# Performance work log

Measured on AMD Instinct MI355X. Metric: run time of the kernel, lower is better.

Reference implementation:

```python
import jax, jax.numpy as jnp
import numpy as np

D_K = 24
ALPHA = 0.1
N_HEADS = 6
D_MODEL = 144
LN_EPS = 1e-5


def setup_inputs() -> dict:
    key = jax.random.key(0)
    ks = jax.random.split(key, 8)
    B, S = 8, 2048
    Q = jax.random.normal(ks[0], (B, S, D_MODEL), dtype=jnp.float32)
    K = jax.random.normal(ks[1], (B, N_HEADS, S, D_K), dtype=jnp.float32)
    V = jax.random.normal(ks[2], (B, N_HEADS, S, D_K), dtype=jnp.float32)
    attn_mask = jax.random.randint(ks[3], (B, S, S), 0, 2).astype(bool)
    Wq_w = jax.random.normal(ks[4], (D_MODEL, D_MODEL), dtype=jnp.float32) * 0.05
    Wq_b = jnp.zeros((D_MODEL,), dtype=jnp.float32)
    lin_w = jax.random.normal(ks[5], (D_MODEL, D_MODEL), dtype=jnp.float32) * 0.05
    lin_b = jnp.zeros((D_MODEL,), dtype=jnp.float32)
    ln_g = jnp.ones((D_MODEL,), dtype=jnp.float32)
    ln_b = jnp.zeros((D_MODEL,), dtype=jnp.float32)
    return {"Q": Q, "K": K, "V": V, "attn_mask": attn_mask,
            "Wq_w": Wq_w, "Wq_b": Wq_b, "lin_w": lin_w, "lin_b": lin_b,
            "ln_g": ln_g, "ln_b": ln_b}


def reference(Q, K, V, attn_mask, Wq_w, Wq_b, lin_w, lin_b, ln_g, ln_b):
    B, S, _ = Q.shape
    residual = Q
    # W_Q projection then head split: [B,S,D] -> [B,H,S,d_k]
    q = (Q @ Wq_w.T + Wq_b).reshape(B, S, N_HEADS, D_K).transpose(0, 2, 1, 3)
    # scores [B,H,S,Sk]; custom tanh activation instead of softmax
    scores = jnp.einsum('bhqd,bhkd->bhqk', q, K) / np.sqrt(D_K).astype(np.float32)
    attn = jnp.tanh(ALPHA * scores)
    # NOTE: original calls attn.masked_fill(...) non-inplace and drops the
    # result, so attn_mask has no effect. Faithfully ignored here.
    context = jnp.einsum('bhqk,bhkd->bhqd', attn, V)
    context = context.transpose(0, 2, 1, 3).reshape(B, S, N_HEADS * D_K)
    output = context @ lin_w.T + lin_b
    x = output + residual
    mu = jnp.mean(x, axis=-1, keepdims=True)
    var = jnp.var(x, axis=-1, keepdims=True)
    return (x - mu) / jnp.sqrt(var + LN_EPS) * ln_g + ln_b
```

## Files before the change

kernel.cpp:

```cpp
#include <hip/hip_runtime.h>
#include <hip/hip_bf16.h>

#define B_  8
#define S_  2048
#define H_  6
#define DK_ 24
#define DM_ 144

#define TK0  2.0412414523193153e-02f
#define TK1 -2.8350575726379381e-06f
#define TK2  4.7250959543965635e-10f

typedef __bf16 bf16x8 __attribute__((ext_vector_type(8)));
typedef __bf16 bf16x2 __attribute__((ext_vector_type(2)));
typedef float  f32x4  __attribute__((ext_vector_type(4)));

#define MFMA_ __builtin_amdgcn_mfma_f32_16x16x32_bf16

__device__ __forceinline__ unsigned short f2bf(float f) {
    return __builtin_bit_cast(unsigned short, (__bf16)f);
}
__device__ __forceinline__ uint pack2(float a, float b) {
    bf16x2 v; v[0] = (__bf16)a; v[1] = (__bf16)b;
    return __builtin_bit_cast(uint, v);
}
__device__ __forceinline__ float tanh_s(float c) {
    float t = c * c;
    float u = fmaf(t, TK2, TK1);
    u = fmaf(t, u, TK0);
    return c * u;
}

__global__ __launch_bounds__(256)
void prep_w_kernel(const float* __restrict__ Wq, const float* __restrict__ Wqb,
                   const float* __restrict__ Wl, const float* __restrict__ lb,
                   ushort* __restrict__ Whq, ushort* __restrict__ Wlp) {
    int i = blockIdx.x * 256 + threadIdx.x;
    if (i < 30720) {
        int h = i / 5120, rem = i % 5120;
        int d = rem / 160, c = rem % 160;
        float v = 0.f;
        if (d < DK_) {
            if (c < DM_)       v = Wq[(h * DK_ + d) * DM_ + c];
            else if (c == DM_) v = Wqb[h * DK_ + d];
        }
        Whq[i] = f2bf(v);
    } else if (i < 53760) {
        int j = i - 30720;
        int r = j / 160, c = j % 160;
        float v = (c < DM_) ? Wl[r * DM_ + c] : (c == DM_ ? lb[r] : 0.f);
        Wlp[j] = f2bf(v);
    }
}

__global__ __launch_bounds__(256)
void prep_kv_kernel(const float* __restrict__ K, const float* __restrict__ V,
                    ushort* __restrict__ Ktt, ushort* __restrict__ Vtt) {
    __shared__ float sv[64 * 25];
    const int t = threadIdx.x;
    const int kt = blockIdx.x, h = blockIdx.y, b = blockIdx.z;
    const int bh = b * H_ + h;
    const size_t tile = (size_t)(bh * 32 + kt);
    const float4* Ks = (const float4*)(K + ((size_t)bh * S_ + kt * 64) * DK_);
    ushort* Ko = Ktt + tile * 2048;
    for (int idx = t; idx < 384; idx += 256) {
        int r = idx / 6, c4 = (idx % 6) * 4;
        float4 v = Ks[idx];
        ushort4 u; u.x = f2bf(v.x); u.y = f2bf(v.y); u.z = f2bf(v.z); u.w = f2bf(v.w);
        *(ushort4*)&Ko[r * 32 + c4] = u;
    }
    if (t < 64) { uint4 z = {0u,0u,0u,0u}; *(uint4*)&Ko[t * 32 + 24] = z; }
    const float4* Vs = (const float4*)(V + ((size_t)bh * S_ + kt * 64) * DK_);
    for (int idx = t; idx < 384; idx += 256) {
        int r = idx / 6, c4 = (idx % 6) * 4;
        *(float4*)&sv[r * 25 + c4] = Vs[idx];
    }
    __syncthreads();
    int d = t >> 3, s8 = (t & 7) * 8;
    uint4 o = {0u,0u,0u,0u};
    if (d < DK_) {
        o.x = pack2(sv[(s8 + 0) * 25 + d], sv[(s8 + 1) * 25 + d]);
        o.y = pack2(sv[(s8 + 2) * 25 + d], sv[(s8 + 3) * 25 + d]);
        o.z = pack2(sv[(s8 + 4) * 25 + d], sv[(s8 + 5) * 25 + d]);
        o.w = pack2(sv[(s8 + 6) * 25 + d], sv[(s8 + 7) * 25 + d]);
    }
    ((uint4*)Vtt)[tile * 256 + t] = o;
}

__global__ __launch_bounds__(512, 6)
void attn_kernel(const float* __restrict__ Q, const ushort* __restrict__ Whq,
                 const ushort* __restrict__ Ktt, const ushort* __restrict__ Vtt,
                 float* __restrict__ out) {
    __shared__ __attribute__((aligned(16))) char smem[48128];
    ushort* s_q  = (ushort*)smem;
    ushort* s_k  = (ushort*)(smem + 10240);
    ushort* s_vt = (ushort*)(smem + 20480);
    ushort* s_p  = (ushort*)(smem + 29696);
    float*  s_ctx = (float*)smem;

    const int t = threadIdx.x;
    const int w = t >> 6, n16 = t & 15, g = (t >> 4) & 3;
    const int qp = blockIdx.x, h = blockIdx.y, b = blockIdx.z;
    const int bh = b * H_ + h;
    const int row0 = qp * 128;

    const uint4* Kb4 = (const uint4*)Ktt + (size_t)bh * 8192;
    const uint4* Vb4 = (const uint4*)Vtt + (size_t)bh * 8192;

    const int t2 = t & 255;
    const int stoff = (t < 256) ? ((t2 >> 2) * 40 + (t2 & 3) * 8)
                                : ((t2 >> 3) * 72 + (t2 & 7) * 8);
    uint4 sreg = (t < 256) ? Kb4[t2] : Vb4[t2];

    const f32x4 zf = {0.f, 0.f, 0.f, 0.f};
    const uint4* Wh4 = (const uint4*)Whq + h * 640;
    {
        const float* Qr = Q + (size_t)(b * S_ + row0 + w * 16 + n16) * DM_;
        f32x4 qa0 = zf, qa1 = zf;
#pragma unroll
        for (int ks = 0; ks < 5; ++ks) {
            bf16x8 av;
            if (ks < 4 || g < 2) {
                float4 f0 = *(const float4*)&Qr[ks * 32 + g * 8];
                float4 f1 = *(const float4*)&Qr[ks * 32 + g * 8 + 4];
                uint4 u;
                u.x = pack2(f0.x, f0.y); u.y = pack2(f0.z, f0.w);
                u.z = pack2(f1.x, f1.y); u.w = pack2(f1.z, f1.w);
                av = __builtin_bit_cast(bf16x8, u);
            } else {
                uint4 u = {0u, 0u, 0u, 0u};
                if (g == 2) u.x = 0x00003F80u;
                av = __builtin_bit_cast(bf16x8, u);
            }
            bf16x8 bv0 = __builtin_bit_cast(bf16x8, Wh4[n16 * 20 + ks * 4 + g]);
            bf16x8 bv1 = __builtin_bit_cast(bf16x8, Wh4[(16 + n16) * 20 + ks * 4 + g]);
            qa0 = MFMA_(av, bv0, qa0, 0, 0, 0);
            qa1 = MFMA_(av, bv1, qa1, 0, 0, 0);
        }
#pragma unroll
        for (int reg = 0; reg < 4; ++reg) {
            int r = (w * 16 + g * 4 + reg) * 40;
            s_q[r + n16]      = f2bf(qa0[reg]);
            s_q[r + 16 + n16] = f2bf(qa1[reg]);
        }
    }
    const bf16x8 qf = *(const bf16x8*)&s_q[(w * 16 + n16) * 40 + g * 8];

    ushort* s_pw = s_p + w * 1152;
    const int prow = n16 * 72;
    f32x4 acc0 = zf, acc1 = zf;
    int p = 0;
    for (int kt = 0; kt < 32; ++kt) {
        if (t < 256) *(uint4*)&s_k[p * 2560 + stoff] = sreg;
        else         *(uint4*)&s_vt[p * 2304 + stoff] = sreg;
        __syncthreads();
        {
            int nt = ((kt + 1) & 31) * 256;
            sreg = (t < 256) ? Kb4[nt + t2] : Vb4[nt + t2];
        }
        bf16x8 a0 = *(const bf16x8*)&s_k[p * 2560 + n16 * 40 + g * 8];
        bf16x8 a1 = *(const bf16x8*)&s_k[p * 2560 + (16 + n16) * 40 + g * 8];
        bf16x8 a2 = *(const bf16x8*)&s_k[p * 2560 + (32 + n16) * 40 + g * 8];
        bf16x8 a3 = *(const bf16x8*)&s_k[p * 2560 + (48 + n16) * 40 + g * 8];
        f32x4 c0 = MFMA_(a0, qf, zf, 0, 0, 0);
        f32x4 c1 = MFMA_(a1, qf, zf, 0, 0, 0);
        f32x4 c2 = MFMA_(a2, qf, zf, 0, 0, 0);
        f32x4 c3 = MFMA_(a3, qf, zf, 0, 0, 0);
        uint2 u;
        u.x = pack2(tanh_s(c0[0]), tanh_s(c0[1]));
        u.y = pack2(tanh_s(c0[2]), tanh_s(c0[3]));
        *(uint2*)&s_pw[prow + 0  + g * 4] = u;
        u.x = pack2(tanh_s(c1[0]), tanh_s(c1[1]));
        u.y = pack2(tanh_s(c1[2]), tanh_s(c1[3]));
        *(uint2*)&s_pw[prow + 16 + g * 4] = u;
        u.x = pack2(tanh_s(c2[0]), tanh_s(c2[1]));
        u.y = pack2(tanh_s(c2[2]), tanh_s(c2[3]));
        *(uint2*)&s_pw[prow + 32 + g * 4] = u;
        u.x = pack2(tanh_s(c3[0]), tanh_s(c3[1]));
        u.y = pack2(tanh_s(c3[2]), tanh_s(c3[3]));
        *(uint2*)&s_pw[prow + 48 + g * 4] = u;
        bf16x8 ap0 = *(const bf16x8*)&s_pw[prow + g * 8];
        bf16x8 ap1 = *(const bf16x8*)&s_pw[prow + 32 + g * 8];
        bf16x8 vb00 = *(const bf16x8*)&s_vt[p * 2304 + n16 * 72 + g * 8];
        bf16x8 vb01 = *(const bf16x8*)&s_vt[p * 2304 + n16 * 72 + 32 + g * 8];
        bf16x8 vb10 = *(const bf16x8*)&s_vt[p * 2304 + (16 + n16) * 72 + g * 8];
        bf16x8 vb11 = *(const bf16x8*)&s_vt[p * 2304 + (16 + n16) * 72 + 32 + g * 8];
        acc0 = MFMA_(ap0, vb00, acc0, 0, 0, 0);
        acc0 = MFMA_(ap1, vb01, acc0, 0, 0, 0);
        acc1 = MFMA_(ap0, vb10, acc1, 0, 0, 0);
        acc1 = MFMA_(ap1, vb11, acc1, 0, 0, 0);
        p ^= 1;
    }

    __syncthreads();
#pragma unroll
    for (int reg = 0; reg < 4; ++reg) {
        int row = w * 16 + g * 4 + reg;
        s_ctx[row * 28 + n16] = acc0[reg];
        if (n16 < 8) s_ctx[row * 28 + 16 + n16] = acc1[reg];
    }
    __syncthreads();
    for (int idx = t; idx < 768; idx += 512) {
        int r = idx / 6, c = idx % 6;
        float4 v4 = *(const float4*)&s_ctx[r * 28 + c * 4];
        *(float4*)&out[((size_t)b * S_ + row0 + r) * DM_ + h * DK_ + c * 4] = v4;
    }
}

__global__ __launch_bounds__(512)
void outln_kernel(const float* __restrict__ Qres, const ushort* __restrict__ Wlp,
                  const float* __restrict__ lg, const float* __restrict__ lbeta,
                  float* __restrict__ io) {
    __shared__ __attribute__((aligned(16))) ushort s_a[64 * 168];
    __shared__ __attribute__((aligned(16))) ushort s_w[144 * 168];
    __shared__ float s_red[2][2][64];
    const int t = threadIdx.x;
    const int w = t >> 6, n16 = t & 15, g = (t >> 4) & 3;
    const int wq = w & 3, half = w >> 2;
    const int nt_base = half * 5, nt_cnt = half ? 4 : 5;
    const int row0 = blockIdx.x * 64;

    for (int idx = t; idx < 2304; idx += 512) {
        int r = idx / 36, c4 = (idx % 36) * 4;
        float4 v = *(const float4*)&io[(size_t)(row0 + r) * DM_ + c4];
        uint2 u; u.x = pack2(v.x, v.y); u.y = pack2(v.z, v.w);
        *(uint2*)&s_a[r * 168 + c4] = u;
    }
    if (t < 64) {
        uint4 pad = {0x00003F80u, 0u, 0u, 0u};
        uint4 z4  = {0u, 0u, 0u, 0u};
        *(uint4*)&s_a[t * 168 + 144] = pad;
        *(uint4*)&s_a[t * 168 + 152] = z4;
    }
    for (int idx = t; idx < 2880; idx += 512) {
        int r = idx / 20, c8 = (idx % 20) * 8;
        *(uint4*)&s_w[r * 168 + c8] = *(const uint4*)&Wlp[r * 160 + c8];
    }
    __syncthreads();

    f32x4 acc[5];
#pragma unroll
    for (int j = 0; j < 5; ++j) acc[j] = (f32x4){0.f, 0.f, 0.f, 0.f};
#pragma unroll
    for (int ks = 0; ks < 5; ++ks) {
        bf16x8 av = *(const bf16x8*)&s_a[(wq * 16 + n16) * 168 + ks * 32 + g * 8];
        for (int j = 0; j < nt_cnt; ++j) {
            bf16x8 bv = *(const bf16x8*)&s_w[((nt_base + j) * 16 + n16) * 168 + ks * 32 + g * 8];
            acc[j] = MFMA_(av, bv, acc[j], 0, 0, 0);
        }
    }
    float vals[5][4], s1[4] = {0, 0, 0, 0}, s2[4] = {0, 0, 0, 0};
    for (int j = 0; j < nt_cnt; ++j) {
        int d = (nt_base + j) * 16 + n16;
#pragma unroll
        for (int reg = 0; reg < 4; ++reg) {
            int row = row0 + wq * 16 + g * 4 + reg;
            float v = acc[j][reg] + Qres[(size_t)row * DM_ + d];
            vals[j][reg] = v;
            s1[reg] += v; s2[reg] = fmaf(v, v, s2[reg]);
        }
    }
#pragma unroll
    for (int off = 1; off < 16; off <<= 1) {
#pragma unroll
        for (int reg = 0; reg < 4; ++reg) {
            s1[reg] += __shfl_xor(s1[reg], off);
            s2[reg] += __shfl_xor(s2[reg], off);
        }
    }
    if (n16 == 0) {
#pragma unroll
        for (int reg = 0; reg < 4; ++reg) {
            int rr = wq * 16 + g * 4 + reg;
            s_red[half][0][rr] = s1[reg];
            s_red[half][1][rr] = s2[reg];
        }
    }
    __syncthreads();
    float mu[4], rs[4];
#pragma unroll
    for (int reg = 0; reg < 4; ++reg) {
        int rr = wq * 16 + g * 4 + reg;
        float S1 = s_red[0][0][rr] + s_red[1][0][rr];
        float S2 = s_red[0][1][rr] + s_red[1][1][rr];
        float m = S1 * (1.f / 144.f);
        mu[reg] = m;
        rs[reg] = rsqrtf(S2 * (1.f / 144.f) - m * m + 1e-5f);
    }
    for (int j = 0; j < nt_cnt; ++j) {
        int d = (nt_base + j) * 16 + n16;
        float gv = lg[d], bv = lbeta[d];
#pragma unroll
        for (int reg = 0; reg < 4; ++reg) {
            int row = row0 + wq * 16 + g * 4 + reg;
            io[(size_t)row * DM_ + d] = (vals[j][reg] - mu[reg]) * rs[reg] * gv + bv;
        }
    }
}

extern "C" void kernel_launch(void* const* d_in, const int* in_sizes, int n_in,
                              void* d_out, int out_size, void* d_ws, size_t ws_size,
                              hipStream_t stream) {
    const float* Q     = (const float*)d_in[0];
    const float* K     = (const float*)d_in[1];
    const float* V     = (const float*)d_in[2];
    const float* Wq_w  = (const float*)d_in[4];
    const float* Wq_b  = (const float*)d_in[5];
    const float* lin_w = (const float*)d_in[6];
    const float* lin_b = (const float*)d_in[7];
    const float* ln_g  = (const float*)d_in[8];
    const float* ln_b  = (const float*)d_in[9];
    float* out = (float*)d_out;

    ushort* Ktt = (ushort*)d_ws;
    ushort* Vtt = (ushort*)((char*)d_ws + 6291456);
    ushort* Whq = (ushort*)((char*)d_ws + 12582912);
    ushort* Wlp = (ushort*)((char*)d_ws + 12644352);

    prep_w_kernel<<<210, 256, 0, stream>>>(Wq_w, Wq_b, lin_w, lin_b, Whq, Wlp);
    prep_kv_kernel<<<dim3(32, H_, B_), 256, 0, stream>>>(K, V, Ktt, Vtt);
    attn_kernel<<<dim3(S_ / 128, H_, B_), 512, 0, stream>>>(Q, Whq, Ktt, Vtt, out);
    outln_kernel<<<(B_ * S_) / 64, 512, 0, stream>>>(Q, Wlp, ln_g, ln_b, out);
}
```

Measured before the change: 268.4 us.

## Split attention key range across waves with LDS atomic reduction, drop shared K/V staging

```diff
diff --git a/kernel.cpp b/kernel.cpp
--- a/kernel.cpp
+++ b/kernel.cpp
@@ -87,32 +87,31 @@
     ((uint4*)Vtt)[tile * 256 + t] = o;
 }
 
-__global__ __launch_bounds__(512, 6)
+__global__ __launch_bounds__(256, 3)
 void attn_kernel(const float* __restrict__ Q, const ushort* __restrict__ Whq,
                  const ushort* __restrict__ Ktt, const ushort* __restrict__ Vtt,
                  float* __restrict__ out) {
-    __shared__ __attribute__((aligned(16))) char smem[48128];
+    __shared__ __attribute__((aligned(16))) char smem[51200];
     ushort* s_q  = (ushort*)smem;
-    ushort* s_k  = (ushort*)(smem + 10240);
-    ushort* s_vt = (ushort*)(smem + 20480);
-    ushort* s_p  = (ushort*)(smem + 29696);
-    float*  s_ctx = (float*)smem;
+    float*  s_ctx = (float*)(smem + 5120);
 
     const int t = threadIdx.x;
     const int w = t >> 6, n16 = t & 15, g = (t >> 4) & 3;
     const int qp = blockIdx.x, h = blockIdx.y, b = blockIdx.z;
     const int bh = b * H_ + h;
-    const int row0 = qp * 128;
+    const int row0 = qp * 64;
 
     const uint4* Kb4 = (const uint4*)Ktt + (size_t)bh * 8192;
     const uint4* Vb4 = (const uint4*)Vtt + (size_t)bh * 8192;
-
-    const int t2 = t & 255;
-    const int stoff = (t < 256) ? ((t2 >> 2) * 40 + (t2 & 3) * 8)
-                                : ((t2 >> 3) * 72 + (t2 & 7) * 8);
-    uint4 sreg = (t < 256) ? Kb4[t2] : Vb4[t2];
-
+    const int koff = n16 * 4 + g;
+    const int voff = n16 * 8 + g;
     const f32x4 zf = {0.f, 0.f, 0.f, 0.f};
+
+    bf16x8 kf[4];
+#pragma unroll
+    for (int mt = 0; mt < 4; ++mt)
+        kf[mt] = __builtin_bit_cast(bf16x8, Kb4[w * 256 + mt * 64 + koff]);
+
     const uint4* Wh4 = (const uint4*)Whq + h * 640;
     {
         const float* Qr = Q + (size_t)(b * S_ + row0 + w * 16 + n16) * DM_;
@@ -144,65 +143,75 @@
             s_q[r + 16 + n16] = f2bf(qa1[reg]);
         }
     }
-    const bf16x8 qf = *(const bf16x8*)&s_q[(w * 16 + n16) * 40 + g * 8];
-
-    ushort* s_pw = s_p + w * 1152;
-    const int prow = n16 * 72;
-    f32x4 acc0 = zf, acc1 = zf;
-    int p = 0;
-    for (int kt = 0; kt < 32; ++kt) {
-        if (t < 256) *(uint4*)&s_k[p * 2560 + stoff] = sreg;
-        else         *(uint4*)&s_vt[p * 2304 + stoff] = sreg;
-        __syncthreads();
+    for (int i = t; i < 2304; i += 256) s_ctx[i] = 0.f;
+    __syncthreads();
+
+    bf16x8 qf[4];
+#pragma unroll
+    for (int j = 0; j < 4; ++j)
+        qf[j] = *(const bf16x8*)&s_q[(j * 16 + n16) * 40 + g * 8];
+
+    ushort* s_pw = (ushort*)(smem + 14336) + w * 4608;
+    f32x4 acc[4][2];
+#pragma unroll
+    for (int m = 0; m < 4; ++m) { acc[m][0] = zf; acc[m][1] = zf; }
+
+    for (int i = 0; i < 8; ++i) {
+        const int kt = i * 4 + w;
+        uint4 vl[4];
+#pragma unroll
+        for (int j = 0; j < 4; ++j)
+            vl[j] = Vb4[kt * 256 + (j >> 1) * 128 + (j & 1) * 4 + voff];
+#pragma unroll
+        for (int mt = 0; mt < 4; ++mt) {
+            f32x4 c0 = MFMA_(kf[mt], qf[0], zf, 0, 0, 0);
+            f32x4 c1 = MFMA_(kf[mt], qf[1], zf, 0, 0, 0);
+            f32x4 c2 = MFMA_(kf[mt], qf[2], zf, 0, 0, 0);
+            f32x4 c3 = MFMA_(kf[mt], qf[3], zf, 0, 0, 0);
+            uint2 u;
+            u.x = pack2(tanh_s(c0[0]), tanh_s(c0[1]));
+            u.y = pack2(tanh_s(c0[2]), tanh_s(c0[3]));
+            *(uint2*)&s_pw[n16 * 72 + mt * 16 + g * 4] = u;
+            u.x = pack2(tanh_s(c1[0]), tanh_s(c1[1]));
+            u.y = pack2(tanh_s(c1[2]), tanh_s(c1[3]));
+            *(uint2*)&s_pw[(16 + n16) * 72 + mt * 16 + g * 4] = u;
+            u.x = pack2(tanh_s(c2[0]), tanh_s(c2[1]));
+            u.y = pack2(tanh_s(c2[2]), tanh_s(c2[3]));
+            *(uint2*)&s_pw[(32 + n16) * 72 + mt * 16 + g * 4] = u;
+            u.x = pack2(tanh_s(c3[0]), tanh_s(c3[1]));
+            u.y = pack2(tanh_s(c3[2]), tanh_s(c3[3]));
+            *(uint2*)&s_pw[(48 + n16) * 72 + mt * 16 + g * 4] = u;
+        }
         {
-            int nt = ((kt + 1) & 31) * 256;
-            sreg = (t < 256) ? Kb4[nt + t2] : Vb4[nt + t2];
-        }
-        bf16x8 a0 = *(const bf16x8*)&s_k[p * 2560 + n16 * 40 + g * 8];
-        bf16x8 a1 = *(const bf16x8*)&s_k[p * 2560 + (16 + n16) * 40 + g * 8];
-        bf16x8 a2 = *(const bf16x8*)&s_k[p * 2560 + (32 + n16) * 40 + g * 8];
-        bf16x8 a3 = *(const bf16x8*)&s_k[p * 2560 + (48 + n16) * 40 + g * 8];
-        f32x4 c0 = MFMA_(a0, qf, zf, 0, 0, 0);
-        f32x4 c1 = MFMA_(a1, qf, zf, 0, 0, 0);
-        f32x4 c2 = MFMA_(a2, qf, zf, 0, 0, 0);
-        f32x4 c3 = MFMA_(a3, qf, zf, 0, 0, 0);
-        uint2 u;
-        u.x = pack2(tanh_s(c0[0]), tanh_s(c0[1]));
-        u.y = pack2(tanh_s(c0[2]), tanh_s(c0[3]));
-        *(uint2*)&s_pw[prow + 0  + g * 4] = u;
-        u.x = pack2(tanh_s(c1[0]), tanh_s(c1[1]));
-        u.y = pack2(tanh_s(c1[2]), tanh_s(c1[3]));
-        *(uint2*)&s_pw[prow + 16 + g * 4] = u;
-        u.x = pack2(tanh_s(c2[0]), tanh_s(c2[1]));
-        u.y = pack2(tanh_s(c2[2]), tanh_s(c2[3]));
-        *(uint2*)&s_pw[prow + 32 + g * 4] = u;
-        u.x = pack2(tanh_s(c3[0]), tanh_s(c3[1]));
-        u.y = pack2(tanh_s(c3[2]), tanh_s(c3[3]));
-        *(uint2*)&s_pw[prow + 48 + g * 4] = u;
-        bf16x8 ap0 = *(const bf16x8*)&s_pw[prow + g * 8];
-        bf16x8 ap1 = *(const bf16x8*)&s_pw[prow + 32 + g * 8];
-        bf16x8 vb00 = *(const bf16x8*)&s_vt[p * 2304 + n16 * 72 + g * 8];
-        bf16x8 vb01 = *(const bf16x8*)&s_vt[p * 2304 + n16 * 72 + 32 + g * 8];
-        bf16x8 vb10 = *(const bf16x8*)&s_vt[p * 2304 + (16 + n16) * 72 + g * 8];
-        bf16x8 vb11 = *(const bf16x8*)&s_vt[p * 2304 + (16 + n16) * 72 + 32 + g * 8];
-        acc0 = MFMA_(ap0, vb00, acc0, 0, 0, 0);
-        acc0 = MFMA_(ap1, vb01, acc0, 0, 0, 0);
-        acc1 = MFMA_(ap0, vb10, acc1, 0, 0, 0);
-        acc1 = MFMA_(ap1, vb11, acc1, 0, 0, 0);
-        p ^= 1;
-    }
-
-    __syncthreads();
-#pragma unroll
-    for (int reg = 0; reg < 4; ++reg) {
-        int row = w * 16 + g * 4 + reg;
-        s_ctx[row * 28 + n16] = acc0[reg];
-        if (n16 < 8) s_ctx[row * 28 + 16 + n16] = acc1[reg];
-    }
-    __syncthreads();
-    for (int idx = t; idx < 768; idx += 512) {
+            const int ktn = (kt + 4) & 31;
+#pragma unroll
+            for (int mt = 0; mt < 4; ++mt)
+                kf[mt] = __builtin_bit_cast(bf16x8, Kb4[ktn * 256 + mt * 64 + koff]);
+        }
+#pragma unroll
+        for (int mt2 = 0; mt2 < 4; ++mt2) {
+            bf16x8 ap0 = *(const bf16x8*)&s_pw[(mt2 * 16 + n16) * 72 + g * 8];
+            bf16x8 ap1 = *(const bf16x8*)&s_pw[(mt2 * 16 + n16) * 72 + 32 + g * 8];
+            acc[mt2][0] = MFMA_(ap0, __builtin_bit_cast(bf16x8, vl[0]), acc[mt2][0], 0, 0, 0);
+            acc[mt2][0] = MFMA_(ap1, __builtin_bit_cast(bf16x8, vl[1]), acc[mt2][0], 0, 0, 0);
+            acc[mt2][1] = MFMA_(ap0, __builtin_bit_cast(bf16x8, vl[2]), acc[mt2][1], 0, 0, 0);
+            acc[mt2][1] = MFMA_(ap1, __builtin_bit_cast(bf16x8, vl[3]), acc[mt2][1], 0, 0, 0);
+        }
+    }
+
+#pragma unroll
+    for (int mt2 = 0; mt2 < 4; ++mt2) {
+#pragma unroll
+        for (int reg = 0; reg < 4; ++reg) {
+            int q = mt2 * 16 + g * 4 + reg;
+            atomicAdd(&s_ctx[q * 36 + n16], acc[mt2][0][reg]);
+            if (n16 < 8) atomicAdd(&s_ctx[q * 36 + 16 + n16], acc[mt2][1][reg]);
+        }
+    }
+    __syncthreads();
+    for (int idx = t; idx < 384; idx += 256) {
         int r = idx / 6, c = idx % 6;
-        float4 v4 = *(const float4*)&s_ctx[r * 28 + c * 4];
+        float4 v4 = *(const float4*)&s_ctx[r * 36 + c * 4];
         *(float4*)&out[((size_t)b * S_ + row0 + r) * DM_ + h * DK_ + c * 4] = v4;
     }
 }
@@ -319,6 +328,6 @@
 
     prep_w_kernel<<<210, 256, 0, stream>>>(Wq_w, Wq_b, lin_w, lin_b, Whq, Wlp);
     prep_kv_kernel<<<dim3(32, H_, B_), 256, 0, stream>>>(K, V, Ktt, Vtt);
-    attn_kernel<<<dim3(S_ / 128, H_, B_), 512, 0, stream>>>(Q, Whq, Ktt, Vtt, out);
+    attn_kernel<<<dim3(S_ / 64, H_, B_), 256, 0, stream>>>(Q, Whq, Ktt, Vtt, out);
     outln_kernel<<<(B_ * S_) / 64, 512, 0, stream>>>(Q, Wlp, ln_g, ln_b, out);
 }
```

After: 295.6 us. +10.1%, slower.

## Restructure attention: 64-row blocks, V fragments in registers, packed fp16 tanh

Applied to the files above, without the earlier changes.

```diff
diff --git a/kernel.cpp b/kernel.cpp
--- a/kernel.cpp
+++ b/kernel.cpp
@@ -6,16 +6,16 @@
 #define H_  6
 #define DK_ 24
 #define DM_ 144
-
-#define TK0  2.0412414523193153e-02f
-#define TK1 -2.8350575726379381e-06f
-#define TK2  4.7250959543965635e-10f
+#define SCALE_ 0.020412414523193153f
 
 typedef __bf16 bf16x8 __attribute__((ext_vector_type(8)));
 typedef __bf16 bf16x2 __attribute__((ext_vector_type(2)));
+typedef _Float16 h16x2 __attribute__((ext_vector_type(2)));
+typedef _Float16 h16x8 __attribute__((ext_vector_type(8)));
 typedef float  f32x4  __attribute__((ext_vector_type(4)));
 
-#define MFMA_ __builtin_amdgcn_mfma_f32_16x16x32_bf16
+#define MFMA_  __builtin_amdgcn_mfma_f32_16x16x32_bf16
+#define MFMAH_ __builtin_amdgcn_mfma_f32_16x16x32_f16
 
 __device__ __forceinline__ unsigned short f2bf(float f) {
     return __builtin_bit_cast(unsigned short, (__bf16)f);
@@ -24,11 +24,19 @@
     bf16x2 v; v[0] = (__bf16)a; v[1] = (__bf16)b;
     return __builtin_bit_cast(uint, v);
 }
-__device__ __forceinline__ float tanh_s(float c) {
-    float t = c * c;
-    float u = fmaf(t, TK2, TK1);
-    u = fmaf(t, u, TK0);
-    return c * u;
+__device__ __forceinline__ uint pkrtz(float a, float b) {
+    return __builtin_bit_cast(uint, __builtin_amdgcn_cvt_pkrtz(a, b));
+}
+__device__ __forceinline__ uint tanh2(float a, float b) {
+    h16x2 x = __builtin_bit_cast(h16x2, __builtin_amdgcn_cvt_pkrtz(a, b));
+    h16x2 t = x * x;
+    const h16x2 c2 = {(_Float16)(2.0f / 15.0f), (_Float16)(2.0f / 15.0f)};
+    const h16x2 c1 = {(_Float16)(-1.0f / 3.0f), (_Float16)(-1.0f / 3.0f)};
+    const h16x2 one = {(_Float16)1.0f, (_Float16)1.0f};
+    h16x2 u = __builtin_elementwise_fma(t, c2, c1);
+    u = __builtin_elementwise_fma(t, u, one);
+    h16x2 r = x * u;
+    return __builtin_bit_cast(uint, r);
 }
 
 __global__ __launch_bounds__(256)
@@ -41,8 +49,8 @@
         int d = rem / 160, c = rem % 160;
         float v = 0.f;
         if (d < DK_) {
-            if (c < DM_)       v = Wq[(h * DK_ + d) * DM_ + c];
-            else if (c == DM_) v = Wqb[h * DK_ + d];
+            if (c < DM_)       v = SCALE_ * Wq[(h * DK_ + d) * DM_ + c];
+            else if (c == DM_) v = SCALE_ * Wqb[h * DK_ + d];
         }
         Whq[i] = f2bf(v);
     } else if (i < 53760) {
@@ -79,40 +87,38 @@
     int d = t >> 3, s8 = (t & 7) * 8;
     uint4 o = {0u,0u,0u,0u};
     if (d < DK_) {
-        o.x = pack2(sv[(s8 + 0) * 25 + d], sv[(s8 + 1) * 25 + d]);
-        o.y = pack2(sv[(s8 + 2) * 25 + d], sv[(s8 + 3) * 25 + d]);
-        o.z = pack2(sv[(s8 + 4) * 25 + d], sv[(s8 + 5) * 25 + d]);
-        o.w = pack2(sv[(s8 + 6) * 25 + d], sv[(s8 + 7) * 25 + d]);
+        o.x = pkrtz(sv[(s8 + 0) * 25 + d], sv[(s8 + 1) * 25 + d]);
+        o.y = pkrtz(sv[(s8 + 2) * 25 + d], sv[(s8 + 3) * 25 + d]);
+        o.z = pkrtz(sv[(s8 + 4) * 25 + d], sv[(s8 + 5) * 25 + d]);
+        o.w = pkrtz(sv[(s8 + 6) * 25 + d], sv[(s8 + 7) * 25 + d]);
     }
     ((uint4*)Vtt)[tile * 256 + t] = o;
 }
 
-__global__ __launch_bounds__(512, 6)
+__global__ __launch_bounds__(256, 6)
 void attn_kernel(const float* __restrict__ Q, const ushort* __restrict__ Whq,
                  const ushort* __restrict__ Ktt, const ushort* __restrict__ Vtt,
                  float* __restrict__ out) {
-    __shared__ __attribute__((aligned(16))) char smem[48128];
-    ushort* s_q  = (ushort*)smem;
-    ushort* s_k  = (ushort*)(smem + 10240);
-    ushort* s_vt = (ushort*)(smem + 20480);
-    ushort* s_p  = (ushort*)(smem + 29696);
+    __shared__ __attribute__((aligned(16))) char smem[24576];
+    ushort* s_q = (ushort*)smem;
+    ushort* s_k = (ushort*)(smem + 5120);
+    ushort* s_p = (ushort*)(smem + 15360);
     float*  s_ctx = (float*)smem;
 
     const int t = threadIdx.x;
     const int w = t >> 6, n16 = t & 15, g = (t >> 4) & 3;
     const int qp = blockIdx.x, h = blockIdx.y, b = blockIdx.z;
     const int bh = b * H_ + h;
-    const int row0 = qp * 128;
+    const int row0 = qp * 64;
 
     const uint4* Kb4 = (const uint4*)Ktt + (size_t)bh * 8192;
     const uint4* Vb4 = (const uint4*)Vtt + (size_t)bh * 8192;
-
-    const int t2 = t & 255;
-    const int stoff = (t < 256) ? ((t2 >> 2) * 40 + (t2 & 3) * 8)
-                                : ((t2 >> 3) * 72 + (t2 & 7) * 8);
-    uint4 sreg = (t < 256) ? Kb4[t2] : Vb4[t2];
-
+    const int stoff = (t >> 2) * 40 + (t & 3) * 8;
+    const int voff = n16 * 8 + g;
     const f32x4 zf = {0.f, 0.f, 0.f, 0.f};
+
+    uint4 kst = Kb4[t];
+
     const uint4* Wh4 = (const uint4*)Whq + h * 640;
     {
         const float* Qr = Q + (size_t)(b * S_ + row0 + w * 16 + n16) * DM_;
@@ -144,55 +150,56 @@
             s_q[r + 16 + n16] = f2bf(qa1[reg]);
         }
     }
-    const bf16x8 qf = *(const bf16x8*)&s_q[(w * 16 + n16) * 40 + g * 8];
-
-    ushort* s_pw = s_p + w * 1152;
-    const int prow = n16 * 72;
+    *(uint4*)&s_k[stoff] = kst;
+    kst = Kb4[256 + t];
+    uint4 vr[4];
+#pragma unroll
+    for (int j = 0; j < 4; ++j)
+        vr[j] = Vb4[(j >> 1) * 128 + (j & 1) * 4 + voff];
+    __syncthreads();
+
+    bf16x8 qf[4];
+#pragma unroll
+    for (int j = 0; j < 4; ++j)
+        qf[j] = *(const bf16x8*)&s_q[(j * 16 + n16) * 40 + g * 8];
+
     f32x4 acc0 = zf, acc1 = zf;
     int p = 0;
     for (int kt = 0; kt < 32; ++kt) {
-        if (t < 256) *(uint4*)&s_k[p * 2560 + stoff] = sreg;
-        else         *(uint4*)&s_vt[p * 2304 + stoff] = sreg;
+        *(uint4*)&s_k[(p ^ 1) * 2560 + stoff] = kst;
+        kst = Kb4[((kt + 2) & 31) * 256 + t];
+        bf16x8 kfrag = *(const bf16x8*)&s_k[p * 2560 + (w * 16 + n16) * 40 + g * 8];
+        f32x4 c0 = MFMA_(kfrag, qf[0], zf, 0, 0, 0);
+        f32x4 c1 = MFMA_(kfrag, qf[1], zf, 0, 0, 0);
+        f32x4 c2 = MFMA_(kfrag, qf[2], zf, 0, 0, 0);
+        f32x4 c3 = MFMA_(kfrag, qf[3], zf, 0, 0, 0);
+        const int pc = w * 16 + g * 4;
+        uint2 u;
+        u.x = tanh2(c0[0], c0[1]); u.y = tanh2(c0[2], c0[3]);
+        *(uint2*)&s_p[(n16) * 72 + pc] = u;
+        u.x = tanh2(c1[0], c1[1]); u.y = tanh2(c1[2], c1[3]);
+        *(uint2*)&s_p[(16 + n16) * 72 + pc] = u;
+        u.x = tanh2(c2[0], c2[1]); u.y = tanh2(c2[2], c2[3]);
+        *(uint2*)&s_p[(32 + n16) * 72 + pc] = u;
+        u.x = tanh2(c3[0], c3[1]); u.y = tanh2(c3[2], c3[3]);
+        *(uint2*)&s_p[(48 + n16) * 72 + pc] = u;
         __syncthreads();
+        h16x8 ap0 = *(const h16x8*)&s_p[(w * 16 + n16) * 72 + g * 8];
+        h16x8 ap1 = *(const h16x8*)&s_p[(w * 16 + n16) * 72 + 32 + g * 8];
+        acc0 = MFMAH_(ap0, __builtin_bit_cast(h16x8, vr[0]), acc0, 0, 0, 0);
+        acc0 = MFMAH_(ap1, __builtin_bit_cast(h16x8, vr[1]), acc0, 0, 0, 0);
+        acc1 = MFMAH_(ap0, __builtin_bit_cast(h16x8, vr[2]), acc1, 0, 0, 0);
+        acc1 = MFMAH_(ap1, __builtin_bit_cast(h16x8, vr[3]), acc1, 0, 0, 0);
         {
-            int nt = ((kt + 1) & 31) * 256;
-            sreg = (t < 256) ? Kb4[nt + t2] : Vb4[nt + t2];
-        }
-        bf16x8 a0 = *(const bf16x8*)&s_k[p * 2560 + n16 * 40 + g * 8];
-        bf16x8 a1 = *(const bf16x8*)&s_k[p * 2560 + (16 + n16) * 40 + g * 8];
-        bf16x8 a2 = *(const bf16x8*)&s_k[p * 2560 + (32 + n16) * 40 + g * 8];
-        bf16x8 a3 = *(const bf16x8*)&s_k[p * 2560 + (48 + n16) * 40 + g * 8];
-        f32x4 c0 = MFMA_(a0, qf, zf, 0, 0, 0);
-        f32x4 c1 = MFMA_(a1, qf, zf, 0, 0, 0);
-        f32x4 c2 = MFMA_(a2, qf, zf, 0, 0, 0);
-        f32x4 c3 = MFMA_(a3, qf, zf, 0, 0, 0);
-        uint2 u;
-        u.x = pack2(tanh_s(c0[0]), tanh_s(c0[1]));
-        u.y = pack2(tanh_s(c0[2]), tanh_s(c0[3]));
-        *(uint2*)&s_pw[prow + 0  + g * 4] = u;
-        u.x = pack2(tanh_s(c1[0]), tanh_s(c1[1]));
-        u.y = pack2(tanh_s(c1[2]), tanh_s(c1[3]));
-        *(uint2*)&s_pw[prow + 16 + g * 4] = u;
-        u.x = pack2(tanh_s(c2[0]), tanh_s(c2[1]));
-        u.y = pack2(tanh_s(c2[2]), tanh_s(c2[3]));
-        *(uint2*)&s_pw[prow + 32 + g * 4] = u;
-        u.x = pack2(tanh_s(c3[0]), tanh_s(c3[1]));
-        u.y = pack2(tanh_s(c3[2]), tanh_s(c3[3]));
-        *(uint2*)&s_pw[prow + 48 + g * 4] = u;
-        bf16x8 ap0 = *(const bf16x8*)&s_pw[prow + g * 8];
-        bf16x8 ap1 = *(const bf16x8*)&s_pw[prow + 32 + g * 8];
-        bf16x8 vb00 = *(const bf16x8*)&s_vt[p * 2304 + n16 * 72 + g * 8];
-        bf16x8 vb01 = *(const bf16x8*)&s_vt[p * 2304 + n16 * 72 + 32 + g * 8];
-        bf16x8 vb10 = *(const bf16x8*)&s_vt[p * 2304 + (16 + n16) * 72 + g * 8];
-        bf16x8 vb11 = *(const bf16x8*)&s_vt[p * 2304 + (16 + n16) * 72 + 32 + g * 8];
-        acc0 = MFMA_(ap0, vb00, acc0, 0, 0, 0);
-        acc0 = MFMA_(ap1, vb01, acc0, 0, 0, 0);
-        acc1 = MFMA_(ap0, vb10, acc1, 0, 0, 0);
-        acc1 = MFMA_(ap1, vb11, acc1, 0, 0, 0);
+            const int tb = ((kt + 1) & 31) * 256;
+#pragma unroll
+            for (int j = 0; j < 4; ++j)
+                vr[j] = Vb4[tb + (j >> 1) * 128 + (j & 1) * 4 + voff];
+        }
         p ^= 1;
-    }
-
-    __syncthreads();
+        __syncthreads();
+    }
+
 #pragma unroll
     for (int reg = 0; reg < 4; ++reg) {
         int row = w * 16 + g * 4 + reg;
@@ -200,7 +207,7 @@
         if (n16 < 8) s_ctx[row * 28 + 16 + n16] = acc1[reg];
     }
     __syncthreads();
-    for (int idx = t; idx < 768; idx += 512) {
+    for (int idx = t; idx < 384; idx += 256) {
         int r = idx / 6, c = idx % 6;
         float4 v4 = *(const float4*)&s_ctx[r * 28 + c * 4];
         *(float4*)&out[((size_t)b * S_ + row0 + r) * DM_ + h * DK_ + c * 4] = v4;
@@ -319,6 +326,6 @@
 
     prep_w_kernel<<<210, 256, 0, stream>>>(Wq_w, Wq_b, lin_w, lin_b, Whq, Wlp);
     prep_kv_kernel<<<dim3(32, H_, B_), 256, 0, stream>>>(K, V, Ktt, Vtt);
-    attn_kernel<<<dim3(S_ / 128, H_, B_), 512, 0, stream>>>(Q, Whq, Ktt, Vtt, out);
+    attn_kernel<<<dim3(S_ / 64, H_, B_), 256, 0, stream>>>(Q, Whq, Ktt, Vtt, out);
     outln_kernel<<<(B_ * S_) / 64, 512, 0, stream>>>(Q, Wlp, ln_g, ln_b, out);
 }
```

Result: slower. 315.5 us (+17.5%).
